# Kernel optimization log

Hardware: AMD Instinct MI355X
Metric: run time of the kernel (lower is better)

The kernel has to match this reference:

```python
import jax, jax.numpy as jnp
import numpy as np

T, H, F, E, K = 2048, 1024, 1024, 8, 2  # tokens, hidden, ffn, experts, top_k


def setup_inputs() -> dict:
    key = jax.random.key(0)
    k1, k2, k3, k4, k5 = jax.random.split(key, 5)
    hidden_states = jax.random.normal(k1, (T, H), dtype=jnp.float32)
    # router outputs: positive weights (renormalize=False in module, used as-is)
    topk_weights = jax.random.uniform(k2, (T, K), dtype=jnp.float32)
    topk_ids = jax.random.randint(k3, (T, K), 0, E, dtype=jnp.int32)
    # gate_up: (E, 2F, H) with first F rows = gate, last F rows = up
    gate_up_weight = jax.random.normal(k4, (E, 2 * F, H), dtype=jnp.float32) * 0.02
    # down: (E, H, F)
    down_weight = jax.random.normal(k5, (E, H, F), dtype=jnp.float32) * 0.02
    return {
        'hidden_states': hidden_states,
        'topk_weights': topk_weights,
        'topk_ids': topk_ids,
        'gate_up_weight': gate_up_weight,
        'down_weight': down_weight,
    }


def reference(hidden_states, topk_weights, topk_ids, gate_up_weight, down_weight):
    # Fused MoE: per selected expert, y = (silu(x@Wg^T) * (x@Wu^T)) @ Wd^T,
    # combined with router weights (renormalize=False).
    f = down_weight.shape[-1]
    # [T, E, 2F]: gate_up projection for every expert (dense ref for grouped GEMM)
    gu = jnp.einsum('th,eoh->teo', hidden_states, gate_up_weight)
    gate, up = gu[..., :f], gu[..., f:]
    act = jax.nn.silu(gate) * up                     # [T, E, F]
    y = jnp.einsum('tef,ehf->teh', act, down_weight)  # [T, E, H]
    # gather the top-k experts per token and combine
    y_sel = jnp.take_along_axis(y, topk_ids[:, :, None], axis=1)  # [T, K, H]
    out = jnp.sum(y_sel * topk_weights[:, :, None], axis=1)       # [T, H]
    return out.astype(hidden_states.dtype)
```

## Files before the change

kernel.cpp:

```cpp
#include <hip/hip_runtime.h>
#include <hip/hip_bf16.h>

#define T_TOK 2048
#define HID   1024
#define FF    1024
#define NEXP  8
#define NPAIR 4096

#define BM 128
#define BK 32
#define MAX_MT 40
#define MAXROWS (MAX_MT*BM)
#define PPT (NPAIR/256)

using bf16x8 = __attribute__((ext_vector_type(8))) __bf16;
using f32x4  = __attribute__((ext_vector_type(4))) float;

__device__ __forceinline__ unsigned short f2bf(float f) {
    unsigned int u = __float_as_uint(f);
    return (unsigned short)((u + 0x7FFF + ((u >> 16) & 1)) >> 16);
}
__device__ __forceinline__ float bf2f(unsigned short s) {
    return __uint_as_float(((unsigned int)s) << 16);
}
__device__ __forceinline__ void gll16(const unsigned short* g, unsigned short* l) {
    __builtin_amdgcn_global_load_lds(
        (const __attribute__((address_space(1))) void*)(const void*)g,
        (__attribute__((address_space(3))) void*)(void*)l, 16, 0, 0);
}

__global__ void prep_kernel(const float* __restrict__ wgu,
                            const float* __restrict__ wdn,
                            const float* __restrict__ hs,
                            const int* __restrict__ ids,
                            int* __restrict__ pair_pos,
                            int* __restrict__ row_tok,
                            int* __restrict__ meta,
                            unsigned short* __restrict__ wgu_b,
                            unsigned short* __restrict__ wdn_b,
                            unsigned short* __restrict__ hs_b) {
    int tid = threadIdx.x;
    if (blockIdx.x == 2048) {
        __shared__ int S[2][256][NEXP];
        __shared__ int base[NEXP];
        int myc[NEXP];
        int eloc[PPT];
#pragma unroll
        for (int e = 0; e < NEXP; e++) myc[e] = 0;
#pragma unroll
        for (int i = 0; i < PPT; i++) {
            int e = ids[tid * PPT + i];
            eloc[i] = e;
#pragma unroll
            for (int ee = 0; ee < NEXP; ee++) myc[ee] += (e == ee);
        }
#pragma unroll
        for (int e = 0; e < NEXP; e++) S[0][tid][e] = myc[e];
        __syncthreads();
        int src = 0;
        for (int d = 1; d < 256; d <<= 1) {
#pragma unroll
            for (int e = 0; e < NEXP; e++) {
                int v = S[src][tid][e];
                if (tid >= d) v += S[src][tid - d][e];
                S[src ^ 1][tid][e] = v;
            }
            __syncthreads();
            src ^= 1;
        }
        if (tid == 0) {
            int mt = 0;
            for (int e = 0; e < NEXP; e++) {
                meta[e] = mt;
                base[e] = mt * BM;
                mt += (S[src][255][e] + BM - 1) / BM;
            }
            meta[NEXP] = mt;
        }
        for (int i = tid; i < MAXROWS; i += 256) row_tok[i] = -1;
        __syncthreads();
        int off[NEXP];
#pragma unroll
        for (int e = 0; e < NEXP; e++) off[e] = base[e] + S[src][tid][e] - myc[e];
#pragma unroll
        for (int i = 0; i < PPT; i++) {
            int p = tid * PPT + i;
            int e = eloc[i];
            int pos = 0;
#pragma unroll
            for (int ee = 0; ee < NEXP; ee++) if (e == ee) pos = off[ee]++;
            pair_pos[p] = pos;
            row_tok[pos] = p >> 1;
        }
        return;
    }
    long stride = 2048L * 256;
    long t0 = (long)blockIdx.x * 256 + tid;
    const long NW1 = (long)NEXP * 2 * FF * HID / 4;
    for (long i = t0; i < NW1; i += stride) {
        float4 v = ((const float4*)wgu)[i];
        ushort4 o; o.x = f2bf(v.x); o.y = f2bf(v.y); o.z = f2bf(v.z); o.w = f2bf(v.w);
        ((ushort4*)wgu_b)[i] = o;
    }
    const long NW2 = (long)NEXP * HID * FF / 4;
    for (long i = t0; i < NW2; i += stride) {
        float4 v = ((const float4*)wdn)[i];
        ushort4 o; o.x = f2bf(v.x); o.y = f2bf(v.y); o.z = f2bf(v.z); o.w = f2bf(v.w);
        ((ushort4*)wdn_b)[i] = o;
    }
    const long NH = (long)T_TOK * HID / 4;
    for (long i = t0; i < NH; i += stride) {
        float4 v = ((const float4*)hs)[i];
        ushort4 o; o.x = f2bf(v.x); o.y = f2bf(v.y); o.z = f2bf(v.z); o.w = f2bf(v.w);
        ((ushort4*)hs_b)[i] = o;
    }
}

template<int EPI, int NBY, int BN>
__global__ __launch_bounds__(256)
void gemm_moe(const unsigned short* __restrict__ A,
              const unsigned short* __restrict__ B,
              unsigned short* __restrict__ Cbf,
              const int* __restrict__ meta,
              const int* __restrict__ row_tok,
              int K, long Bexp) {
    constexpr int NJ = BN / 32;
    constexpr int NBCH = (BN * BK) / (8 * 256);
    __shared__ unsigned short As[2][BM * BK];
    __shared__ unsigned short Bs[2][BN * BK];

    int L = blockIdx.x;
    int xcd = L & 7;
    int slot = L >> 3;
    constexpr int PER = NBY / 8;
    int by = xcd * PER + (slot % PER);
    int bx = slot / PER;
    if (bx >= meta[NEXP]) return;
    int e = 0;
#pragma unroll
    for (int i = 1; i < NEXP; i++) if (bx >= meta[i]) e = i;

    long m0 = (long)bx * BM;
    int n0 = by * BN;
    const unsigned short* Bb = B + (long)e * Bexp;

    int tid = threadIdx.x, lane = tid & 63, wv = tid >> 6;
    const int r = lane & 15;
    const int q = lane >> 4;
    const int mw = (wv >> 1) * 64, nw = (wv & 1) * (BN / 2);
    const int sw = (q ^ ((r >> 1) & 3)) * 8;

    const unsigned short* ap[2];
#pragma unroll
    for (int h = 0; h < 2; h++) {
        int c = h * 256 + tid;
        int row = c >> 2, cp = c & 3;
        int cc = cp ^ ((row >> 1) & 3);
        long grow;
        if (EPI == 1) {
            int tk = row_tok[m0 + row];
            if (tk < 0) tk = 0;
            grow = tk;
        } else {
            grow = m0 + row;
        }
        ap[h] = A + grow * (long)K + cc * 8;
    }
    const unsigned short* bp[NBCH];
#pragma unroll
    for (int h = 0; h < NBCH; h++) {
        int c = h * 256 + tid;
        int row = c >> 2, cp = c & 3;
        int cc = cp ^ ((row >> 1) & 3);
        long grow;
        if (EPI == 1) grow = ((row & 1) ? FF : 0) + ((n0 + row) >> 1);
        else          grow = n0 + row;
        bp[h] = Bb + grow * (long)K + cc * 8;
    }

    auto stage = [&](int s, int k0) {
#pragma unroll
        for (int h = 0; h < 2; h++)
            gll16(ap[h] + k0, &As[s][(h * 256 + tid) * 8]);
#pragma unroll
        for (int h = 0; h < NBCH; h++)
            gll16(bp[h] + k0, &Bs[s][(h * 256 + tid) * 8]);
    };

    f32x4 acc[4][NJ] = {};
    const int NKI = K / BK;
    stage(0, 0);
    for (int ki = 0; ki < NKI; ki++) {
        __syncthreads();
        if (ki + 1 < NKI) stage((ki + 1) & 1, (ki + 1) * BK);
        int s = ki & 1;
        bf16x8 a[4], b[NJ];
#pragma unroll
        for (int i = 0; i < 4; i++)
            a[i] = *(const bf16x8*)&As[s][(mw + i * 16 + r) * BK + sw];
#pragma unroll
        for (int j = 0; j < NJ; j++)
            b[j] = *(const bf16x8*)&Bs[s][(nw + j * 16 + r) * BK + sw];
#pragma unroll
        for (int i = 0; i < 4; i++)
#pragma unroll
            for (int j = 0; j < NJ; j++)
                acc[i][j] = __builtin_amdgcn_mfma_f32_16x16x32_bf16(a[i], b[j], acc[i][j], 0, 0, 0);
        __syncthreads();
    }

    if (EPI == 1) {
#pragma unroll
        for (int i = 0; i < 4; i++) {
            long rowb = m0 + mw + i * 16 + q * 4;
#pragma unroll
            for (int j = 0; j < NJ; j++) {
                int n = n0 + nw + j * 16 + r;
#pragma unroll
                for (int reg = 0; reg < 4; reg++) {
                    float v = acc[i][j][reg];
                    float o = __shfl_xor(v, 1);
                    if (!(r & 1)) {
                        float g = v, u = o;
                        float s2 = g / (1.f + __expf(-g)) * u;
                        Cbf[(rowb + reg) * (long)FF + (n >> 1)] = f2bf(s2);
                    }
                }
            }
        }
    } else {
#pragma unroll
        for (int i = 0; i < 4; i++) {
            long rowb = m0 + mw + i * 16 + q * 4;
#pragma unroll
            for (int j = 0; j < NJ; j++) {
                int n = n0 + nw + j * 16 + r;
#pragma unroll
                for (int reg = 0; reg < 4; reg++)
                    Cbf[(rowb + reg) * (long)HID + n] = f2bf(acc[i][j][reg]);
            }
        }
    }
}

__global__ void combine_kernel(const unsigned short* __restrict__ y,
                               const float* __restrict__ tw,
                               const int* __restrict__ pair_pos,
                               float* __restrict__ out) {
    int t = blockIdx.x;
    int c = threadIdx.x * 4;
    int p0 = pair_pos[t * 2], p1 = pair_pos[t * 2 + 1];
    float w0 = tw[t * 2], w1 = tw[t * 2 + 1];
    ushort4 a = *(const ushort4*)(y + (long)p0 * HID + c);
    ushort4 b = *(const ushort4*)(y + (long)p1 * HID + c);
    float4 o;
    o.x = w0 * bf2f(a.x) + w1 * bf2f(b.x);
    o.y = w0 * bf2f(a.y) + w1 * bf2f(b.y);
    o.z = w0 * bf2f(a.z) + w1 * bf2f(b.z);
    o.w = w0 * bf2f(a.w) + w1 * bf2f(b.w);
    *(float4*)(out + (long)t * HID + c) = o;
}

extern "C" void kernel_launch(void* const* d_in, const int* in_sizes, int n_in,
                              void* d_out, int out_size, void* d_ws, size_t ws_size,
                              hipStream_t stream) {
    const float* hs  = (const float*)d_in[0];
    const float* tw  = (const float*)d_in[1];
    const int*   ids = (const int*)d_in[2];
    const float* wgu = (const float*)d_in[3];
    const float* wdn = (const float*)d_in[4];
    float* out = (float*)d_out;

    char* ws = (char*)d_ws;
    size_t off = 0;
    auto alloc = [&](size_t bytes) -> void* {
        void* p = ws + off;
        off += (bytes + 255) & ~(size_t)255;
        return p;
    };
    unsigned short* wgu_b = (unsigned short*)alloc((size_t)NEXP * 2 * FF * HID * 2);
    unsigned short* wdn_b = (unsigned short*)alloc((size_t)NEXP * HID * FF * 2);
    unsigned short* hs_b  = (unsigned short*)alloc((size_t)T_TOK * HID * 2);
    unsigned short* act   = (unsigned short*)alloc((size_t)MAXROWS * FF * 2);
    unsigned short* ybuf  = (unsigned short*)alloc((size_t)MAXROWS * HID * 2);
    int* pair_pos = (int*)alloc(NPAIR * 4);
    int* row_tok  = (int*)alloc(MAXROWS * 4);
    int* meta     = (int*)alloc(64);

    prep_kernel<<<2049, 256, 0, stream>>>(wgu, wdn, hs, ids,
                                          pair_pos, row_tok, meta,
                                          wgu_b, wdn_b, hs_b);

    gemm_moe<1, 16, 128><<<16 * MAX_MT, 256, 0, stream>>>(
        hs_b, wgu_b, act, meta, row_tok, HID, (long)(2 * FF) * HID);

    gemm_moe<2, 8, 128><<<8 * MAX_MT, 256, 0, stream>>>(
        act, wdn_b, ybuf, meta, row_tok, FF, (long)HID * FF);

    combine_kernel<<<T_TOK, 256, 0, stream>>>(ybuf, tw, pair_pos, out);
}
```

Before: 203.5 us.

## Triple-buffer GEMM LDS stages with vmcnt waits and restructure the conversion prep kernel

The GEMM main loop moves from a double-buffered LDS ring with two __syncthreads per iteration to a three-stage ring. It waits with explicit s_waitcnt vmcnt and a single barrier, so global-to-LDS loads run two tiles ahead and overlap MFMA work. The prep kernel now gives each block a fixed slice of one conversion array and issues 8 independent float4 loads per thread, replacing the grid-stride loops, which should increase memory-level parallelism. This costs 50% more LDS per block, and correctness depends on the hardcoded vmcnt immediates matching exactly 4 loads per stage. It also drops the trailing barrier before a buffer is overwritten and relies on the three-slot rotation to keep that safe.

```diff
diff --git a/kernel.cpp b/kernel.cpp
--- a/kernel.cpp
+++ b/kernel.cpp
@@ -28,6 +28,15 @@
         (const __attribute__((address_space(1))) void*)(const void*)g,
         (__attribute__((address_space(3))) void*)(void*)l, 16, 0, 0);
 }
+__device__ __forceinline__ ushort4 cvt4(float4 v) {
+    ushort4 o; o.x = f2bf(v.x); o.y = f2bf(v.y); o.z = f2bf(v.z); o.w = f2bf(v.w);
+    return o;
+}
+
+#define B_WGU 2048
+#define B_WDN 1024
+#define B_HS  256
+#define B_TOT (B_WGU + B_WDN + B_HS)
 
 __global__ void prep_kernel(const float* __restrict__ wgu,
                             const float* __restrict__ wdn,
@@ -40,79 +49,78 @@
                             unsigned short* __restrict__ wdn_b,
                             unsigned short* __restrict__ hs_b) {
     int tid = threadIdx.x;
-    if (blockIdx.x == 2048) {
-        __shared__ int S[2][256][NEXP];
-        __shared__ int base[NEXP];
-        int myc[NEXP];
-        int eloc[PPT];
-#pragma unroll
-        for (int e = 0; e < NEXP; e++) myc[e] = 0;
-#pragma unroll
-        for (int i = 0; i < PPT; i++) {
-            int e = ids[tid * PPT + i];
-            eloc[i] = e;
-#pragma unroll
-            for (int ee = 0; ee < NEXP; ee++) myc[ee] += (e == ee);
-        }
-#pragma unroll
-        for (int e = 0; e < NEXP; e++) S[0][tid][e] = myc[e];
+    int bid = blockIdx.x;
+    if (bid < B_TOT) {
+        const float4* src;
+        ushort4* dst;
+        long base;
+        if (bid < B_WGU) {
+            src = (const float4*)wgu; dst = (ushort4*)wgu_b;
+            base = (long)bid * 2048 + tid;
+        } else if (bid < B_WGU + B_WDN) {
+            src = (const float4*)wdn; dst = (ushort4*)wdn_b;
+            base = (long)(bid - B_WGU) * 2048 + tid;
+        } else {
+            src = (const float4*)hs; dst = (ushort4*)hs_b;
+            base = (long)(bid - B_WGU - B_WDN) * 2048 + tid;
+        }
+        float4 v[8];
+#pragma unroll
+        for (int k = 0; k < 8; k++) v[k] = src[base + k * 256];
+#pragma unroll
+        for (int k = 0; k < 8; k++) dst[base + k * 256] = cvt4(v[k]);
+        return;
+    }
+    __shared__ int S[2][256][NEXP];
+    __shared__ int base[NEXP];
+    int myc[NEXP];
+    int eloc[PPT];
+#pragma unroll
+    for (int e = 0; e < NEXP; e++) myc[e] = 0;
+#pragma unroll
+    for (int i = 0; i < PPT; i++) {
+        int e = ids[tid * PPT + i];
+        eloc[i] = e;
+#pragma unroll
+        for (int ee = 0; ee < NEXP; ee++) myc[ee] += (e == ee);
+    }
+#pragma unroll
+    for (int e = 0; e < NEXP; e++) S[0][tid][e] = myc[e];
+    __syncthreads();
+    int src = 0;
+    for (int d = 1; d < 256; d <<= 1) {
+#pragma unroll
+        for (int e = 0; e < NEXP; e++) {
+            int v = S[src][tid][e];
+            if (tid >= d) v += S[src][tid - d][e];
+            S[src ^ 1][tid][e] = v;
+        }
         __syncthreads();
-        int src = 0;
-        for (int d = 1; d < 256; d <<= 1) {
-#pragma unroll
-            for (int e = 0; e < NEXP; e++) {
-                int v = S[src][tid][e];
-                if (tid >= d) v += S[src][tid - d][e];
-                S[src ^ 1][tid][e] = v;
-            }
-            __syncthreads();
-            src ^= 1;
-        }
-        if (tid == 0) {
-            int mt = 0;
-            for (int e = 0; e < NEXP; e++) {
-                meta[e] = mt;
-                base[e] = mt * BM;
-                mt += (S[src][255][e] + BM - 1) / BM;
-            }
-            meta[NEXP] = mt;
-        }
-        for (int i = tid; i < MAXROWS; i += 256) row_tok[i] = -1;
-        __syncthreads();
-        int off[NEXP];
-#pragma unroll
-        for (int e = 0; e < NEXP; e++) off[e] = base[e] + S[src][tid][e] - myc[e];
-#pragma unroll
-        for (int i = 0; i < PPT; i++) {
-            int p = tid * PPT + i;
-            int e = eloc[i];
-            int pos = 0;
-#pragma unroll
-            for (int ee = 0; ee < NEXP; ee++) if (e == ee) pos = off[ee]++;
-            pair_pos[p] = pos;
-            row_tok[pos] = p >> 1;
-        }
-        return;
-    }
-    long stride = 2048L * 256;
-    long t0 = (long)blockIdx.x * 256 + tid;
-    const long NW1 = (long)NEXP * 2 * FF * HID / 4;
-    for (long i = t0; i < NW1; i += stride) {
-        float4 v = ((const float4*)wgu)[i];
-        ushort4 o; o.x = f2bf(v.x); o.y = f2bf(v.y); o.z = f2bf(v.z); o.w = f2bf(v.w);
-        ((ushort4*)wgu_b)[i] = o;
-    }
-    const long NW2 = (long)NEXP * HID * FF / 4;
-    for (long i = t0; i < NW2; i += stride) {
-        float4 v = ((const float4*)wdn)[i];
-        ushort4 o; o.x = f2bf(v.x); o.y = f2bf(v.y); o.z = f2bf(v.z); o.w = f2bf(v.w);
-        ((ushort4*)wdn_b)[i] = o;
-    }
-    const long NH = (long)T_TOK * HID / 4;
-    for (long i = t0; i < NH; i += stride) {
-        float4 v = ((const float4*)hs)[i];
-        ushort4 o; o.x = f2bf(v.x); o.y = f2bf(v.y); o.z = f2bf(v.z); o.w = f2bf(v.w);
-        ((ushort4*)hs_b)[i] = o;
+        src ^= 1;
+    }
+    if (tid == 0) {
+        int mt = 0;
+        for (int e = 0; e < NEXP; e++) {
+            meta[e] = mt;
+            base[e] = mt * BM;
+            mt += (S[src][255][e] + BM - 1) / BM;
+        }
+        meta[NEXP] = mt;
+    }
+    for (int i = tid; i < MAXROWS; i += 256) row_tok[i] = -1;
+    __syncthreads();
+    int off[NEXP];
+#pragma unroll
+    for (int e = 0; e < NEXP; e++) off[e] = base[e] + S[src][tid][e] - myc[e];
+#pragma unroll
+    for (int i = 0; i < PPT; i++) {
+        int p = tid * PPT + i;
+        int e = eloc[i];
+        int pos = 0;
+#pragma unroll
+        for (int ee = 0; ee < NEXP; ee++) if (e == ee) pos = off[ee]++;
+        pair_pos[p] = pos;
+        row_tok[pos] = p >> 1;
     }
 }
 
@@ -125,10 +133,13 @@
               const int* __restrict__ row_tok,
               int K, long Bexp) {
     constexpr int NJ = BN / 32;
+    constexpr int ACH = (BM * BK) / (8 * 256);
     constexpr int NBCH = (BN * BK) / (8 * 256);
-    __shared__ unsigned short As[2][BM * BK];
-    __shared__ unsigned short Bs[2][BN * BK];
-
+    static_assert(ACH + NBCH == 4, "vmcnt immediates assume 4 loads per stage");
+    __shared__ unsigned short As[3][BM * BK];
+    __shared__ unsigned short Bs[3][BN * BK];
+
+    int tid = threadIdx.x;
     int L = blockIdx.x;
     int xcd = L & 7;
     int slot = L >> 3;
@@ -144,15 +155,15 @@
     int n0 = by * BN;
     const unsigned short* Bb = B + (long)e * Bexp;
 
-    int tid = threadIdx.x, lane = tid & 63, wv = tid >> 6;
+    int lane = tid & 63, wv = tid >> 6;
     const int r = lane & 15;
     const int q = lane >> 4;
     const int mw = (wv >> 1) * 64, nw = (wv & 1) * (BN / 2);
     const int sw = (q ^ ((r >> 1) & 3)) * 8;
 
-    const unsigned short* ap[2];
-#pragma unroll
-    for (int h = 0; h < 2; h++) {
+    const unsigned short* ap[ACH];
+#pragma unroll
+    for (int h = 0; h < ACH; h++) {
         int c = h * 256 + tid;
         int row = c >> 2, cp = c & 3;
         int cc = cp ^ ((row >> 1) & 3);
@@ -180,7 +191,7 @@
 
     auto stage = [&](int s, int k0) {
 #pragma unroll
-        for (int h = 0; h < 2; h++)
+        for (int h = 0; h < ACH; h++)
             gll16(ap[h] + k0, &As[s][(h * 256 + tid) * 8]);
 #pragma unroll
         for (int h = 0; h < NBCH; h++)
@@ -190,23 +201,30 @@
     f32x4 acc[4][NJ] = {};
     const int NKI = K / BK;
     stage(0, 0);
+    stage(1, BK);
+    int sb = 0;
     for (int ki = 0; ki < NKI; ki++) {
-        __syncthreads();
-        if (ki + 1 < NKI) stage((ki + 1) & 1, (ki + 1) * BK);
-        int s = ki & 1;
+        if (ki + 1 < NKI) asm volatile("s_waitcnt vmcnt(4)" ::: "memory");
+        else              asm volatile("s_waitcnt vmcnt(0)" ::: "memory");
+        __builtin_amdgcn_s_barrier();
+        __builtin_amdgcn_sched_barrier(0);
+        if (ki + 2 < NKI) {
+            int sn = sb + 2; if (sn >= 3) sn -= 3;
+            stage(sn, (ki + 2) * BK);
+        }
         bf16x8 a[4], b[NJ];
 #pragma unroll
         for (int i = 0; i < 4; i++)
-            a[i] = *(const bf16x8*)&As[s][(mw + i * 16 + r) * BK + sw];
+            a[i] = *(const bf16x8*)&As[sb][(mw + i * 16 + r) * BK + sw];
 #pragma unroll
         for (int j = 0; j < NJ; j++)
-            b[j] = *(const bf16x8*)&Bs[s][(nw + j * 16 + r) * BK + sw];
+            b[j] = *(const bf16x8*)&Bs[sb][(nw + j * 16 + r) * BK + sw];
 #pragma unroll
         for (int i = 0; i < 4; i++)
 #pragma unroll
             for (int j = 0; j < NJ; j++)
                 acc[i][j] = __builtin_amdgcn_mfma_f32_16x16x32_bf16(a[i], b[j], acc[i][j], 0, 0, 0);
-        __syncthreads();
+        sb = (sb == 2) ? 0 : sb + 1;
     }
 
     if (EPI == 1) {
@@ -287,9 +305,9 @@
     int* row_tok  = (int*)alloc(MAXROWS * 4);
     int* meta     = (int*)alloc(64);
 
-    prep_kernel<<<2049, 256, 0, stream>>>(wgu, wdn, hs, ids,
-                                          pair_pos, row_tok, meta,
-                                          wgu_b, wdn_b, hs_b);
+    prep_kernel<<<B_TOT + 1, 256, 0, stream>>>(wgu, wdn, hs, ids,
+                                               pair_pos, row_tok, meta,
+                                               wgu_b, wdn_b, hs_b);
 
     gemm_moe<1, 16, 128><<<16 * MAX_MT, 256, 0, stream>>>(
         hs_b, wgu_b, act, meta, row_tok, HID, (long)(2 * FF) * HID);
```

After: 207.5 us. About the same (+1.9%).
